# Optimization experiments

Measured on AMD Instinct MI355X. Metric: run time of the kernel, lower is better.

## Reference

```python
import jax, jax.numpy as jnp
import numpy as np

GROUPS = 32
EPS = 1e-6


def group_norm(x, scale, bias):
    b, c, h, w = x.shape
    xg = x.reshape(b, GROUPS, c // GROUPS, h, w)
    mean = xg.mean(axis=(2, 3, 4), keepdims=True)
    var = xg.var(axis=(2, 3, 4), keepdims=True)
    xg = (xg - mean) * jax.lax.rsqrt(var + EPS)
    x = xg.reshape(b, c, h, w)
    return x * scale[None, :, None, None] + bias[None, :, None, None]


def conv1x1(x, w, b):
    # x: [B,C,H,W], w: [O,C], b: [O]
    return jnp.einsum('bchw,oc->bohw', x, w) + b[None, :, None, None]


def setup_inputs() -> dict:
    key = jax.random.key(0)
    ks = jax.random.split(key, 11)
    B, C, H, W = 4, 512, 64, 64
    s = 1.0 / np.sqrt(C)
    return {
        'x': jax.random.normal(ks[0], (B, C, H, W), jnp.float32),
        'gn_scale': jnp.ones((C,), jnp.float32),
        'gn_bias': jnp.zeros((C,), jnp.float32),
        'wq': jax.random.normal(ks[1], (C, C), jnp.float32) * s,
        'bq': jnp.zeros((C,), jnp.float32),
        'wk': jax.random.normal(ks[2], (C, C), jnp.float32) * s,
        'bk': jnp.zeros((C,), jnp.float32),
        'wv': jax.random.normal(ks[3], (C, C), jnp.float32) * s,
        'bv': jnp.zeros((C,), jnp.float32),
        'wp': jax.random.normal(ks[4], (C, C), jnp.float32) * s,
        'bp': jnp.zeros((C,), jnp.float32),
    }


def reference(x, gn_scale, gn_bias, wq, bq, wk, bk, wv, bv, wp, bp):
    b, c, h, w = x.shape
    h_ = group_norm(x, gn_scale, gn_bias)
    q = conv1x1(h_, wq, bq).reshape(b, c, h * w)  # [B,C,N]
    k = conv1x1(h_, wk, bk).reshape(b, c, h * w)
    v = conv1x1(h_, wv, bv).reshape(b, c, h * w)
    # scores[b,i,j] = sum_c q[b,c,i]*k[b,c,j] / sqrt(c)
    scores = jnp.einsum('bci,bcj->bij', q, k) * (c ** -0.5)
    attn = jax.nn.softmax(scores, axis=2)
    # out[b,c,i] = sum_j attn[b,i,j] * v[b,c,j]
    out = jnp.einsum('bij,bcj->bci', attn, v).reshape(b, c, h, w)
    out = conv1x1(out, wp, bp)
    return x + out
```

## Files before the change

kernel.cpp:

```cpp
#include <hip/hip_runtime.h>

#define CDIM 512
#define NDIM 4096
#define BATCH 4

using bf8v = __attribute__((ext_vector_type(8))) __bf16;
using f4v  = __attribute__((ext_vector_type(4))) float;

typedef __attribute__((address_space(1))) unsigned int gu32;
typedef __attribute__((address_space(3))) unsigned int lu32;

static __device__ __forceinline__ unsigned short f2bf(float f) {
  unsigned int u = __float_as_uint(f);
  u += 0x7fffu + ((u >> 16) & 1u);
  return (unsigned short)(u >> 16);
}

__global__ __launch_bounds__(256) void gn_stats_kernel(
    const float* __restrict__ x, float* __restrict__ stats) {
  const int tid = threadIdx.x;
  const float4* xv = (const float4*)(x + (long)blockIdx.x * 65536);
  float s = 0.f, ss = 0.f;
  for (int i = tid; i < 16384; i += 256) {
    float4 d = xv[i];
    s  += d.x + d.y + d.z + d.w;
    ss += d.x * d.x + d.y * d.y + d.z * d.z + d.w * d.w;
  }
#pragma unroll
  for (int off = 32; off; off >>= 1) {
    s  += __shfl_down(s, off);
    ss += __shfl_down(ss, off);
  }
  __shared__ float red[8];
  if ((tid & 63) == 0) { red[tid >> 6] = s; red[4 + (tid >> 6)] = ss; }
  __syncthreads();
  if (tid == 0) {
    float S  = red[0] + red[1] + red[2] + red[3];
    float SS = red[4] + red[5] + red[6] + red[7];
    float mean = S * (1.f / 65536.f);
    float var  = SS * (1.f / 65536.f) - mean * mean;
    stats[blockIdx.x * 2]     = mean;
    stats[blockIdx.x * 2 + 1] = rsqrtf(var + 1e-6f);
  }
}

__global__ __launch_bounds__(256) void gn_transpose_kernel(
    const float* __restrict__ x, const float* __restrict__ gs,
    const float* __restrict__ gb, const float* __restrict__ stats,
    unsigned short* __restrict__ hT) {
  __shared__ float t[64][65];
  const int tid = threadIdx.x;
  const int b = blockIdx.z;
  const long bbx = (long)b * ((long)CDIM * NDIM);
  const int n0 = blockIdx.x * 64, c0 = blockIdx.y * 64;
  for (int k = 0; k < 4; ++k) {
    int it = tid + k * 256;
    int c = it >> 4, no = (it & 15) << 2;
    int ch = c0 + c;
    int g = ch >> 4;
    float mean = stats[(b * 32 + g) * 2];
    float rstd = stats[(b * 32 + g) * 2 + 1];
    float a  = rstd * gs[ch];
    float bb = gb[ch] - mean * a;
    float4 d = *(const float4*)&x[bbx + (long)ch * NDIM + n0 + no];
    t[no + 0][c] = d.x * a + bb;
    t[no + 1][c] = d.y * a + bb;
    t[no + 2][c] = d.z * a + bb;
    t[no + 3][c] = d.w * a + bb;
  }
  __syncthreads();
  const long bbh = (long)b * ((long)NDIM * CDIM);
  for (int k = 0; k < 2; ++k) {
    int it = tid + k * 256;
    int n = it >> 3, co = (it & 7) << 3;
    unsigned int ow[4];
#pragma unroll
    for (int j = 0; j < 4; ++j) {
      unsigned short lo = f2bf(t[n][co + 2 * j]);
      unsigned short hi = f2bf(t[n][co + 2 * j + 1]);
      ow[j] = (unsigned int)lo | ((unsigned int)hi << 16);
    }
    uint4 o; o.x = ow[0]; o.y = ow[1]; o.z = ow[2]; o.w = ow[3];
    *(uint4*)&hT[bbh + (long)(n0 + n) * CDIM + c0 + co] = o;
  }
}

__global__ __launch_bounds__(256) void prep_kernel(
    const float* __restrict__ wq, const float* __restrict__ wk,
    const float* __restrict__ wv, const float* __restrict__ bq,
    const float* __restrict__ bk, unsigned short* __restrict__ wqkb,
    unsigned short* __restrict__ wvb, float* __restrict__ bqk) {
  int blk = blockIdx.x;
  if (blk < 768) {
    int i = blk * 256 + threadIdx.x;
    const float* src = (blk < 256) ? wq : (blk < 512) ? wk : wv;
    unsigned short* dst = (blk < 256) ? wqkb : (blk < 512) ? (wqkb + 262144) : wvb;
    int j = i - ((blk < 256) ? 0 : (blk < 512) ? 65536 : 131072);
    float4 d = ((const float4*)src)[j];
    ushort4 o;
    o.x = f2bf(d.x); o.y = f2bf(d.y); o.z = f2bf(d.z); o.w = f2bf(d.w);
    ((ushort4*)dst)[j] = o;
  } else {
#pragma unroll
    for (int k = 0; k < 4; ++k) {
      int i = threadIdx.x + k * 256;
      bqk[i] = (i < 512) ? bq[i] : bk[i - 512];
    }
  }
}

__global__ __launch_bounds__(256) void cvt_kernel(
    const float* __restrict__ src, unsigned short* __restrict__ dst, int n4) {
  int i = blockIdx.x * 256 + threadIdx.x;
  if (i >= n4) return;
  float4 d = ((const float4*)src)[i];
  ushort4 o;
  o.x = f2bf(d.x); o.y = f2bf(d.y); o.z = f2bf(d.z); o.w = f2bf(d.w);
  ((ushort4*)dst)[i] = o;
}

#define BM 128
#define BN 128
#define BK 64

template <int EPI, int SWZ>
__global__ __launch_bounds__(256) void gemm_nt(
    const unsigned short* __restrict__ A, long sA, int lA,
    const unsigned short* __restrict__ B, long sB, int lB,
    void* __restrict__ Cp, long sC,
    const float* __restrict__ bias,
    const float* __restrict__ X, long sX,
    int Nn, int K) {
  __shared__ unsigned short As[BM * BK];
  __shared__ unsigned short Bs[BN * BK];
  int bx, by, bz;
  if (SWZ == 0) {
    bx = blockIdx.x; by = blockIdx.y; bz = blockIdx.z;
  } else if (SWZ == 1) {
    int flat = blockIdx.x;
    int q = flat >> 5, r = flat & 31;
    bx = r >> 3;
    int g = q * 8 + (r & 7);
    by = g & 31; bz = g >> 5;
  } else {
    int flat = blockIdx.x;
    bz = flat >> 10;
    int f = flat & 1023;
    by = (f & 7) + ((f >> 8) << 3);
    bx = (f >> 3) & 31;
  }
  const int tid = threadIdx.x;
  A += (long)bz * sA;
  B += (long)bz * sB;
  const int m0 = by * BM;
  const int n0 = bx * BN;
  const int lane = tid & 63;
  const int wv = tid >> 6;
  const int wm = (wv >> 1) << 6;
  const int wn = (wv & 1) << 6;
  const int l16 = lane & 15;
  const int quad = lane >> 4;
  const int sw = l16 & 7;
  const int r8 = lane >> 3;
  const int c8 = lane & 7;
  const int csw = (c8 ^ r8) << 3;

  f4v acc[4][4] = {};
  f4v accr[4] = {};
  bf8v ones;
#pragma unroll
  for (int i = 0; i < 8; ++i) ones[i] = (__bf16)1.0f;

  const unsigned short* Ag = A + (long)(m0 + wv * 32 + r8) * lA + csw;
  const unsigned short* Bg = B + (long)(n0 + wv * 32 + r8) * lB + csw;
  unsigned short* Asl = As + wv * 32 * BK;
  unsigned short* Bsl = Bs + wv * 32 * BK;

  for (int k0 = 0; k0 < K; k0 += BK) {
#pragma unroll
    for (int i = 0; i < 4; ++i) {
      __builtin_amdgcn_global_load_lds((const gu32*)(Ag + (long)i * 8 * lA + k0),
          (lu32*)(Asl + i * 512), 16, 0, 0);
      __builtin_amdgcn_global_load_lds((const gu32*)(Bg + (long)i * 8 * lB + k0),
          (lu32*)(Bsl + i * 512), 16, 0, 0);
    }
    __syncthreads();
    bf8v af[2][4], bf[2][4];
#pragma unroll
    for (int kk = 0; kk < 2; ++kk) {
#pragma unroll
      for (int t = 0; t < 4; ++t) {
        int ra = wm + t * 16 + l16;
        int rb = wn + t * 16 + l16;
        af[kk][t] = *(const bf8v*)&As[ra * BK + ((((kk << 2) + quad) ^ sw) << 3)];
        bf[kk][t] = *(const bf8v*)&Bs[rb * BK + ((((kk << 2) + quad) ^ sw) << 3)];
      }
    }
#pragma unroll
    for (int kk = 0; kk < 2; ++kk) {
#pragma unroll
      for (int tm = 0; tm < 4; ++tm) {
#pragma unroll
        for (int tn = 0; tn < 4; ++tn)
          acc[tm][tn] = __builtin_amdgcn_mfma_f32_16x16x32_bf16(
              af[kk][tm], bf[kk][tn], acc[tm][tn], 0, 0, 0);
        if (EPI == 3)
          accr[tm] = __builtin_amdgcn_mfma_f32_16x16x32_bf16(
              af[kk][tm], ones, accr[tm], 0, 0, 0);
      }
    }
    __syncthreads();
  }

  if (EPI == 2) {
#pragma unroll
    for (int tm = 0; tm < 4; ++tm) {
#pragma unroll
      for (int r = 0; r < 4; ++r) {
        const int row = m0 + wm + tm * 16 + quad * 4 + r;
#pragma unroll
        for (int tn = 0; tn < 4; ++tn) {
          const int col = n0 + wn + tn * 16 + l16;
          float e = __expf(acc[tm][tn][r] * 0.044194173824159216f);
          ((unsigned short*)Cp)[(long)bz * sC + (long)row * Nn + col] = f2bf(e);
        }
      }
    }
  } else if (EPI == 3) {
#pragma unroll
    for (int tm = 0; tm < 4; ++tm) {
#pragma unroll
      for (int r = 0; r < 4; ++r) {
        const int row = m0 + wm + tm * 16 + quad * 4 + r;
        const float inv = 1.0f / accr[tm][r];
#pragma unroll
        for (int tn = 0; tn < 4; ++tn) {
          const int col = n0 + wn + tn * 16 + l16;
          ((unsigned short*)Cp)[(long)bz * sC + (long)row * Nn + col] =
              f2bf(acc[tm][tn][r] * inv);
        }
      }
    }
  } else {
#pragma unroll
    for (int tm = 0; tm < 4; ++tm) {
#pragma unroll
      for (int tn = 0; tn < 4; ++tn) {
        const int col = n0 + wn + tn * 16 + l16;
#pragma unroll
        for (int r = 0; r < 4; ++r) {
          const int row = m0 + wm + tm * 16 + quad * 4 + r;
          float val = acc[tm][tn][r];
          if (EPI == 0) {
            val += bias[col];
            ((unsigned short*)Cp)[(long)bz * sC + (long)row * Nn + col] = f2bf(val);
          } else if (EPI == 1) {
            val += bias[row];
            ((unsigned short*)Cp)[(long)bz * sC + (long)row * Nn + col] = f2bf(val);
          } else {
            ((float*)Cp)[(long)bz * sC + (long)row * Nn + col] =
                val + bias[row] + X[(long)bz * sX + (long)row * Nn + col];
          }
        }
      }
    }
  }
}

extern "C" void kernel_launch(void* const* d_in, const int* in_sizes, int n_in,
                              void* d_out, int out_size, void* d_ws, size_t ws_size,
                              hipStream_t stream) {
  (void)in_sizes; (void)n_in; (void)out_size;
  const float* x  = (const float*)d_in[0];
  const float* gs = (const float*)d_in[1];
  const float* gb = (const float*)d_in[2];
  const float* wq = (const float*)d_in[3];
  const float* bq = (const float*)d_in[4];
  const float* wk = (const float*)d_in[5];
  const float* bk = (const float*)d_in[6];
  const float* wv = (const float*)d_in[7];
  const float* bv = (const float*)d_in[8];
  const float* wp = (const float*)d_in[9];
  const float* bp = (const float*)d_in[10];
  float* out = (float*)d_out;

  char* ws = (char*)d_ws;
  const long NC  = (long)NDIM * CDIM;
  const long NQK = (long)NDIM * 1024;
  const long BUF = NC * 2 * BATCH;
  const long NN  = (long)NDIM * NDIM;

  unsigned short* hT   = (unsigned short*)(ws);
  unsigned short* OT   = hT;
  unsigned short* qkT  = (unsigned short*)(ws + BUF);
  unsigned short* vB   = (unsigned short*)(ws + BUF * 3);
  unsigned short* sc   = (unsigned short*)(ws + BUF * 4);
  unsigned short* wqkb = sc;
  unsigned short* wvb  = (unsigned short*)(ws + BUF * 4 + 1048576);
  float* bqk           = (float*)(ws + BUF * 4 + 1572864);
  float* stats         = (float*)(ws + BUF * 4 + 1581056);
  unsigned short* wpb  = qkT;

  gn_stats_kernel<<<BATCH * 32, 256, 0, stream>>>(x, stats);
  gn_transpose_kernel<<<dim3(NDIM / 64, CDIM / 64, BATCH), 256, 0, stream>>>(x, gs, gb, stats, hT);
  prep_kernel<<<769, 256, 0, stream>>>(wq, wk, wv, bq, bk, wqkb, wvb, bqk);

  gemm_nt<0, 0><<<dim3(1024 / BN, NDIM / BM, BATCH), 256, 0, stream>>>(
      hT, NC, CDIM, wqkb, 0, CDIM, qkT, NQK, bqk, nullptr, 0, 1024, CDIM);
  gemm_nt<1, 0><<<dim3(NDIM / BN, CDIM / BM, BATCH), 256, 0, stream>>>(
      wvb, 0, CDIM, hT, NC, CDIM, vB, NC, bv, nullptr, 0, NDIM, CDIM);

  if (ws_size >= (size_t)(BUF * 4) + (size_t)(NN * 2) * BATCH) {
    gemm_nt<2, 2><<<dim3(1024 * BATCH, 1, 1), 256, 0, stream>>>(
        qkT, NQK, 1024, qkT + 512, NQK, 1024, sc, NN, nullptr, nullptr, 0, NDIM, CDIM);
    gemm_nt<3, 1><<<dim3(512, 1, 1), 256, 0, stream>>>(
        sc, NN, NDIM, vB, NC, NDIM, OT, NC, nullptr, nullptr, 0, CDIM, NDIM);
  } else {
    for (int b = 0; b < BATCH; ++b) {
      gemm_nt<2, 2><<<dim3(1024, 1, 1), 256, 0, stream>>>(
          qkT + b * NQK, 0, 1024, qkT + b * NQK + 512, 0, 1024, sc, 0,
          nullptr, nullptr, 0, NDIM, CDIM);
      gemm_nt<3, 1><<<dim3(128, 1, 1), 256, 0, stream>>>(
          sc, 0, NDIM, vB + b * NC, 0, NDIM, OT + b * NC, 0,
          nullptr, nullptr, 0, CDIM, NDIM);
    }
  }

  cvt_kernel<<<256, 256, 0, stream>>>(wp, wpb, 65536);
  gemm_nt<4, 0><<<dim3(NDIM / BN, CDIM / BM, BATCH), 256, 0, stream>>>(
      wpb, 0, CDIM, OT, NC, CDIM, out, NC, bp, x, NC, NDIM, CDIM);
}
```

Before: 397.0 us.

## Replace GEMM with 8-wave multi-stage pipelined kernel using larger tiles

Replaces the 256-thread 128x128 GEMM with a templated 512-thread kernel using 256x256 or 128x256 tiles. The K loop now runs a 4-buffer ring of 32-wide K chunks in LDS, prefetching three chunks ahead. It uses explicit vmcnt waits, split barriers and s_setprio around the MFMA groups so global-to-LDS loads overlap with compute. Blocks are reordered with an XCD-aware remap for better L2 locality. This is meant to hide memory latency and raise data reuse, at the cost of more registers and LDS per block and more fragile hand-written wait counts.

```diff
diff --git a/kernel.cpp b/kernel.cpp
--- a/kernel.cpp
+++ b/kernel.cpp
@@ -119,107 +119,139 @@
   ((ushort4*)dst)[i] = o;
 }
 
-#define BM 128
-#define BN 128
-#define BK 64
-
-template <int EPI, int SWZ>
-__global__ __launch_bounds__(256) void gemm_nt(
+template <int BM, int BN, int EPI, int ORD>
+__global__ __launch_bounds__(512, 2) void gemm8(
     const unsigned short* __restrict__ A, long sA, int lA,
     const unsigned short* __restrict__ B, long sB, int lB,
     void* __restrict__ Cp, long sC,
     const float* __restrict__ bias,
     const float* __restrict__ X, long sX,
-    int Nn, int K) {
-  __shared__ unsigned short As[BM * BK];
-  __shared__ unsigned short Bs[BN * BK];
+    int GX, int GY, int Nn, int K) {
+  constexpr int TM = BM / 32;
+  constexpr int TN = BN / 64;
+  constexpr int LA = BM / 128;
+  constexpr int LB = BN / 128;
+  constexpr int VN = 2 * (LA + LB);
+
+  __shared__ __align__(16) unsigned short As[4 * BM * 32];
+  __shared__ __align__(16) unsigned short Bs[4 * BN * 32];
+
+  const int tid = threadIdx.x;
+  const int nwg = gridDim.x;
+  const int g = (blockIdx.x & 7) * (nwg >> 3) + (blockIdx.x >> 3);
   int bx, by, bz;
-  if (SWZ == 0) {
-    bx = blockIdx.x; by = blockIdx.y; bz = blockIdx.z;
-  } else if (SWZ == 1) {
-    int flat = blockIdx.x;
-    int q = flat >> 5, r = flat & 31;
-    bx = r >> 3;
-    int g = q * 8 + (r & 7);
-    by = g & 31; bz = g >> 5;
-  } else {
-    int flat = blockIdx.x;
-    bz = flat >> 10;
-    int f = flat & 1023;
-    by = (f & 7) + ((f >> 8) << 3);
-    bx = (f >> 3) & 31;
-  }
-  const int tid = threadIdx.x;
+  if (ORD == 0) { bx = g % GX; int t = g / GX; by = t % GY; bz = t / GY; }
+  else          { by = g % GY; int t = g / GY; bx = t % GX; bz = t / GX; }
+
   A += (long)bz * sA;
   B += (long)bz * sB;
   const int m0 = by * BM;
   const int n0 = bx * BN;
   const int lane = tid & 63;
   const int wv = tid >> 6;
-  const int wm = (wv >> 1) << 6;
-  const int wn = (wv & 1) << 6;
+  const int wm = (wv >> 2) * (BM / 2);
+  const int wn = (wv & 3) * (BN / 4);
   const int l16 = lane & 15;
   const int quad = lane >> 4;
-  const int sw = l16 & 7;
-  const int r8 = lane >> 3;
-  const int c8 = lane & 7;
-  const int csw = (c8 ^ r8) << 3;
-
-  f4v acc[4][4] = {};
-  f4v accr[4] = {};
+  const int rdo = ((quad ^ (l16 & 3)) << 3);
+
+  const int rl = tid >> 2;
+  const int gl = tid & 3;
+  const int swl = ((gl ^ (rl & 3)) << 3);
+  const unsigned short* Ag = A + (long)(m0 + rl) * lA + swl;
+  const unsigned short* Bg = B + (long)(n0 + rl) * lB + swl;
+  unsigned short* Asl = As + wv * 512;
+  unsigned short* Bsl = Bs + wv * 512;
+
+  const int nchunk = K >> 5;
+
+  auto stageA = [&](int c) {
+    if (c < nchunk) {
+#pragma unroll
+      for (int i = 0; i < LA; ++i)
+        __builtin_amdgcn_global_load_lds(
+            (const gu32*)(Ag + (long)i * 128 * lA + c * 32),
+            (lu32*)(Asl + (c & 3) * (BM * 32) + i * 4096), 16, 0, 0);
+    }
+  };
+  auto stageB = [&](int c) {
+    if (c < nchunk) {
+#pragma unroll
+      for (int i = 0; i < LB; ++i)
+        __builtin_amdgcn_global_load_lds(
+            (const gu32*)(Bg + (long)i * 128 * lB + c * 32),
+            (lu32*)(Bsl + (c & 3) * (BN * 32) + i * 4096), 16, 0, 0);
+    }
+  };
+
+  f4v acc[TM][TN] = {};
+  f4v accr[TM] = {};
   bf8v ones;
 #pragma unroll
   for (int i = 0; i < 8; ++i) ones[i] = (__bf16)1.0f;
 
-  const unsigned short* Ag = A + (long)(m0 + wv * 32 + r8) * lA + csw;
-  const unsigned short* Bg = B + (long)(n0 + wv * 32 + r8) * lB + csw;
-  unsigned short* Asl = As + wv * 32 * BK;
-  unsigned short* Bsl = Bs + wv * 32 * BK;
-
-  for (int k0 = 0; k0 < K; k0 += BK) {
-#pragma unroll
-    for (int i = 0; i < 4; ++i) {
-      __builtin_amdgcn_global_load_lds((const gu32*)(Ag + (long)i * 8 * lA + k0),
-          (lu32*)(Asl + i * 512), 16, 0, 0);
-      __builtin_amdgcn_global_load_lds((const gu32*)(Bg + (long)i * 8 * lB + k0),
-          (lu32*)(Bsl + i * 512), 16, 0, 0);
-    }
-    __syncthreads();
-    bf8v af[2][4], bf[2][4];
-#pragma unroll
-    for (int kk = 0; kk < 2; ++kk) {
-#pragma unroll
-      for (int t = 0; t < 4; ++t) {
-        int ra = wm + t * 16 + l16;
-        int rb = wn + t * 16 + l16;
-        af[kk][t] = *(const bf8v*)&As[ra * BK + ((((kk << 2) + quad) ^ sw) << 3)];
-        bf[kk][t] = *(const bf8v*)&Bs[rb * BK + ((((kk << 2) + quad) ^ sw) << 3)];
-      }
-    }
-#pragma unroll
-    for (int kk = 0; kk < 2; ++kk) {
-#pragma unroll
-      for (int tm = 0; tm < 4; ++tm) {
-#pragma unroll
-        for (int tn = 0; tn < 4; ++tn)
-          acc[tm][tn] = __builtin_amdgcn_mfma_f32_16x16x32_bf16(
-              af[kk][tm], bf[kk][tn], acc[tm][tn], 0, 0, 0);
-        if (EPI == 3)
-          accr[tm] = __builtin_amdgcn_mfma_f32_16x16x32_bf16(
-              af[kk][tm], ones, accr[tm], 0, 0, 0);
-      }
-    }
-    __syncthreads();
-  }
+  auto body = [&](int d) {
+    __builtin_amdgcn_s_barrier();
+    stageA(d + 3);
+    const unsigned short* Ab = As + (d & 3) * (BM * 32);
+    const unsigned short* Bb = Bs + (d & 3) * (BN * 32);
+    bf8v af[TM], bf[TN];
+#pragma unroll
+    for (int t = 0; t < TM; ++t)
+      af[t] = *(const bf8v*)&Ab[(wm + t * 16 + l16) * 32 + rdo];
+#pragma unroll
+    for (int t = 0; t < TN; ++t)
+      bf[t] = *(const bf8v*)&Bb[(wn + t * 16 + l16) * 32 + rdo];
+    __builtin_amdgcn_s_setprio(1);
+#pragma unroll
+    for (int tm = 0; tm < TM / 2; ++tm) {
+#pragma unroll
+      for (int tn = 0; tn < TN; ++tn)
+        acc[tm][tn] = __builtin_amdgcn_mfma_f32_16x16x32_bf16(
+            af[tm], bf[tn], acc[tm][tn], 0, 0, 0);
+      if (EPI == 3)
+        accr[tm] = __builtin_amdgcn_mfma_f32_16x16x32_bf16(
+            af[tm], ones, accr[tm], 0, 0, 0);
+    }
+    __builtin_amdgcn_s_setprio(0);
+    __builtin_amdgcn_s_barrier();
+    stageB(d + 3);
+    __builtin_amdgcn_s_setprio(1);
+#pragma unroll
+    for (int tm = TM / 2; tm < TM; ++tm) {
+#pragma unroll
+      for (int tn = 0; tn < TN; ++tn)
+        acc[tm][tn] = __builtin_amdgcn_mfma_f32_16x16x32_bf16(
+            af[tm], bf[tn], acc[tm][tn], 0, 0, 0);
+      if (EPI == 3)
+        accr[tm] = __builtin_amdgcn_mfma_f32_16x16x32_bf16(
+            af[tm], ones, accr[tm], 0, 0, 0);
+    }
+    __builtin_amdgcn_s_setprio(0);
+  };
+
+  stageA(0); stageB(0); stageA(1); stageB(1); stageA(2); stageB(2);
+
+  int d = 0;
+  for (; d < nchunk - 2; ++d) {
+    if constexpr (VN == 8) asm volatile("s_waitcnt vmcnt(8)" ::: "memory");
+    else                   asm volatile("s_waitcnt vmcnt(6)" ::: "memory");
+    body(d);
+  }
+  if constexpr (VN == 8) asm volatile("s_waitcnt vmcnt(4)" ::: "memory");
+  else                   asm volatile("s_waitcnt vmcnt(3)" ::: "memory");
+  body(d); ++d;
+  asm volatile("s_waitcnt vmcnt(0)" ::: "memory");
+  body(d);
 
   if (EPI == 2) {
 #pragma unroll
-    for (int tm = 0; tm < 4; ++tm) {
+    for (int tm = 0; tm < TM; ++tm) {
 #pragma unroll
       for (int r = 0; r < 4; ++r) {
         const int row = m0 + wm + tm * 16 + quad * 4 + r;
 #pragma unroll
-        for (int tn = 0; tn < 4; ++tn) {
+        for (int tn = 0; tn < TN; ++tn) {
           const int col = n0 + wn + tn * 16 + l16;
           float e = __expf(acc[tm][tn][r] * 0.044194173824159216f);
           ((unsigned short*)Cp)[(long)bz * sC + (long)row * Nn + col] = f2bf(e);
@@ -228,13 +260,13 @@
     }
   } else if (EPI == 3) {
 #pragma unroll
-    for (int tm = 0; tm < 4; ++tm) {
+    for (int tm = 0; tm < TM; ++tm) {
 #pragma unroll
       for (int r = 0; r < 4; ++r) {
         const int row = m0 + wm + tm * 16 + quad * 4 + r;
         const float inv = 1.0f / accr[tm][r];
 #pragma unroll
-        for (int tn = 0; tn < 4; ++tn) {
+        for (int tn = 0; tn < TN; ++tn) {
           const int col = n0 + wn + tn * 16 + l16;
           ((unsigned short*)Cp)[(long)bz * sC + (long)row * Nn + col] =
               f2bf(acc[tm][tn][r] * inv);
@@ -243,9 +275,9 @@
     }
   } else {
 #pragma unroll
-    for (int tm = 0; tm < 4; ++tm) {
-#pragma unroll
-      for (int tn = 0; tn < 4; ++tn) {
+    for (int tm = 0; tm < TM; ++tm) {
+#pragma unroll
+      for (int tn = 0; tn < TN; ++tn) {
         const int col = n0 + wn + tn * 16 + l16;
 #pragma unroll
         for (int r = 0; r < 4; ++r) {
@@ -305,28 +337,30 @@
   gn_transpose_kernel<<<dim3(NDIM / 64, CDIM / 64, BATCH), 256, 0, stream>>>(x, gs, gb, stats, hT);
   prep_kernel<<<769, 256, 0, stream>>>(wq, wk, wv, bq, bk, wqkb, wvb, bqk);
 
-  gemm_nt<0, 0><<<dim3(1024 / BN, NDIM / BM, BATCH), 256, 0, stream>>>(
-      hT, NC, CDIM, wqkb, 0, CDIM, qkT, NQK, bqk, nullptr, 0, 1024, CDIM);
-  gemm_nt<1, 0><<<dim3(NDIM / BN, CDIM / BM, BATCH), 256, 0, stream>>>(
-      wvb, 0, CDIM, hT, NC, CDIM, vB, NC, bv, nullptr, 0, NDIM, CDIM);
+  gemm8<256, 256, 0, 0><<<256, 512, 0, stream>>>(
+      hT, NC, CDIM, wqkb, 0, CDIM, qkT, NQK, bqk, nullptr, 0, 4, 16, 1024, CDIM);
+  gemm8<128, 256, 1, 1><<<256, 512, 0, stream>>>(
+      wvb, 0, CDIM, hT, NC, CDIM, vB, NC, bv, nullptr, 0, 16, 4, NDIM, CDIM);
 
   if (ws_size >= (size_t)(BUF * 4) + (size_t)(NN * 2) * BATCH) {
-    gemm_nt<2, 2><<<dim3(1024 * BATCH, 1, 1), 256, 0, stream>>>(
-        qkT, NQK, 1024, qkT + 512, NQK, 1024, sc, NN, nullptr, nullptr, 0, NDIM, CDIM);
-    gemm_nt<3, 1><<<dim3(512, 1, 1), 256, 0, stream>>>(
-        sc, NN, NDIM, vB, NC, NDIM, OT, NC, nullptr, nullptr, 0, CDIM, NDIM);
+    gemm8<256, 256, 2, 0><<<1024, 512, 0, stream>>>(
+        qkT, NQK, 1024, qkT + 512, NQK, 1024, sc, NN, nullptr, nullptr, 0,
+        16, 16, NDIM, CDIM);
+    gemm8<128, 256, 3, 1><<<256, 512, 0, stream>>>(
+        sc, NN, NDIM, vB, NC, NDIM, OT, NC, nullptr, nullptr, 0,
+        2, 32, CDIM, NDIM);
   } else {
     for (int b = 0; b < BATCH; ++b) {
-      gemm_nt<2, 2><<<dim3(1024, 1, 1), 256, 0, stream>>>(
+      gemm8<256, 256, 2, 0><<<256, 512, 0, stream>>>(
           qkT + b * NQK, 0, 1024, qkT + b * NQK + 512, 0, 1024, sc, 0,
-          nullptr, nullptr, 0, NDIM, CDIM);
-      gemm_nt<3, 1><<<dim3(128, 1, 1), 256, 0, stream>>>(
+          nullptr, nullptr, 0, 16, 16, NDIM, CDIM);
+      gemm8<128, 256, 3, 1><<<64, 512, 0, stream>>>(
           sc, 0, NDIM, vB + b * NC, 0, NDIM, OT + b * NC, 0,
-          nullptr, nullptr, 0, CDIM, NDIM);
+          nullptr, nullptr, 0, 2, 32, CDIM, NDIM);
     }
   }
 
   cvt_kernel<<<256, 256, 0, stream>>>(wp, wpb, 65536);
-  gemm_nt<4, 0><<<dim3(NDIM / BN, CDIM / BM, BATCH), 256, 0, stream>>>(
-      wpb, 0, CDIM, OT, NC, CDIM, out, NC, bp, x, NC, NDIM, CDIM);
-}
+  gemm8<128, 256, 4, 1><<<256, 512, 0, stream>>>(
+      wpb, 0, CDIM, OT, NC, CDIM, out, NC, bp, x, NC, 16, 4, NDIM, CDIM);
+}
```

Measured after the change: 427.0 us. +7.6%, slower.
